# Optimization experiments

Measured on AMD Instinct MI355X. Metric: run time of the kernel, lower is better.

## Reference

```python
import jax, jax.numpy as jnp
import numpy as np

B, T, A, H, E = 256, 64, 32, 512, 32


def setup_inputs() -> dict:
    key = jax.random.key(0)
    ks = jax.random.split(key, 8)
    return {
        "actions": jax.random.normal(ks[0], (B, T, A), dtype=jnp.float32),
        "timesteps": jax.random.randint(ks[1], (B,), 0, 1000, dtype=jnp.int32),
        "cat_ids": jax.random.randint(ks[2], (B,), 0, E, dtype=jnp.int32),
        "W1": 0.02 * jax.random.normal(ks[3], (E, A, H), dtype=jnp.float32),
        "b1": jnp.zeros((E, H), dtype=jnp.float32),
        "W2": 0.02 * jax.random.normal(ks[4], (E, 2 * H, H), dtype=jnp.float32),
        "b2": jnp.zeros((E, H), dtype=jnp.float32),
        "W3": 0.02 * jax.random.normal(ks[5], (E, H, H), dtype=jnp.float32),
        "b3": jnp.zeros((E, H), dtype=jnp.float32),
    }


def _cat_linear(x, cat_ids, W, b):
    # per-sample weight gather + bmm, faithful to torch W[cat_ids]; bmm
    return jnp.einsum("btd,bdh->bth", x, W[cat_ids]) + b[cat_ids][:, None, :]


def _sinusoidal(timesteps_bt, dim):
    half = dim // 2
    exponent = -jnp.arange(half, dtype=jnp.float32) * (jnp.log(jnp.float32(10000.0)) / half)
    freqs = timesteps_bt[..., None] * jnp.exp(exponent)  # (B,T,half)
    return jnp.concatenate([jnp.sin(freqs), jnp.cos(freqs)], axis=-1)


def _swish(x):
    return x * jax.nn.sigmoid(x)


def reference(actions, timesteps, cat_ids, W1, b1, W2, b2, W3, b3):
    Bb, Tt, _ = actions.shape
    t_bt = jnp.broadcast_to(timesteps.astype(jnp.float32)[:, None], (Bb, Tt))
    a_emb = _cat_linear(actions, cat_ids, W1, b1)                     # (B,T,H)
    tau_emb = _sinusoidal(t_bt, a_emb.shape[-1]).astype(a_emb.dtype)  # (B,T,H)
    x = jnp.concatenate([a_emb, tau_emb], axis=-1)                    # (B,T,2H)
    x = _swish(_cat_linear(x, cat_ids, W2, b2))
    return _cat_linear(x, cat_ids, W3, b3)
```

## Files before the change

kernel.cpp:

```cpp
#include <hip/hip_runtime.h>
#include <hip/hip_bf16.h>

#define NB 256
#define NT 64
#define NA 32
#define NH 512
#define NE 32
#define MAXTILES 144

typedef short short8 __attribute__((ext_vector_type(8)));
typedef unsigned short ushort8v __attribute__((ext_vector_type(8)));
typedef float f32x4 __attribute__((ext_vector_type(4)));

__device__ __forceinline__ unsigned short f2bf(float f) {
  unsigned int u = __float_as_uint(f);
  u += 0x7FFFu + ((u >> 16) & 1u);
  return (unsigned short)(u >> 16);
}

__device__ __forceinline__ void gl2lds16(const void* g, void* l) {
  __builtin_amdgcn_global_load_lds(
      (const __attribute__((address_space(1))) unsigned int*)g,
      (__attribute__((address_space(3))) unsigned int*)l, 16, 0, 0);
}

__device__ __forceinline__ ushort8v cvt8(float4 a, float4 b) {
  ushort8v t;
  t[0] = f2bf(a.x); t[1] = f2bf(a.y); t[2] = f2bf(a.z); t[3] = f2bf(a.w);
  t[4] = f2bf(b.x); t[5] = f2bf(b.y); t[6] = f2bf(b.z); t[7] = f2bf(b.w);
  return t;
}

__global__ __launch_bounds__(256) void groupk(const int* __restrict__ cat,
                                              int* __restrict__ tiles,
                                              int* __restrict__ ntiles_out,
                                              int* __restrict__ orderG,
                                              int* __restrict__ offG,
                                              int* __restrict__ cntG) {
  __shared__ int cnt[NE], off[NE], cur[NE];
  __shared__ int order[NB];
  int tid = threadIdx.x;
  if (tid < NE) cnt[tid] = 0;
  __syncthreads();
  int e = cat[tid];
  atomicAdd(&cnt[e], 1);
  __syncthreads();
  if (tid == 0) {
    int s = 0;
    for (int i = 0; i < NE; i++) { off[i] = s; cur[i] = s; s += cnt[i]; }
  }
  __syncthreads();
  int p = atomicAdd(&cur[e], 1);
  order[p] = tid;
  __syncthreads();
  orderG[tid] = order[tid];
  if (tid < NE) { offG[tid] = off[tid]; cntG[tid] = cnt[tid]; }
  if (tid == 0) {
    int nt = 0;
    for (int i = 0; i < NE; i++) {
      for (int j = 0; j < cnt[i]; j += 2) {
        tiles[3 * nt + 0] = i;
        tiles[3 * nt + 1] = order[off[i] + j];
        tiles[3 * nt + 2] = (j + 1 < cnt[i]) ? order[off[i] + j + 1] : -1;
        nt++;
      }
    }
    *ntiles_out = nt;
  }
}

__global__ __launch_bounds__(256) void prep_kernel(const float* __restrict__ W,
                                                   unsigned short* __restrict__ Wt,
                                                   int K) {
  __shared__ float S[64 * 66];
  int e = blockIdx.z;
  int nt = blockIdx.x * 64;
  int kt = blockIdx.y * 64;
  int TK = (K - kt) < 64 ? (K - kt) : 64;
  int tid = threadIdx.x;
  int units = TK * 32;
  for (int u = tid; u < units; u += 256) {
    int k = u >> 5, c = u & 31;
    float2 v = *(const float2*)(W + ((size_t)e * K + kt + k) * NH + nt + 2 * c);
    *(float2*)(&S[k * 66 + 2 * c]) = v;
  }
  __syncthreads();
  int csh = (TK == 64) ? 3 : 2;
  int CHm = (1 << csh) - 1;
  int wunits = 64 << csh;
  for (int u = tid; u < wunits; u += 256) {
    int n = u >> csh, c = u & CHm;
    ushort8v pk;
#pragma unroll
    for (int j = 0; j < 8; j++) pk[j] = f2bf(S[(c * 8 + j) * 66 + n]);
    *(ushort8v*)(Wt + ((size_t)e * NH + nt + n) * K + kt + c * 8) = pk;
  }
}

__device__ __forceinline__ void pf_w2(float2 (&pf)[8], const float* __restrict__ W2en,
                                      int k0, int tid) {
#pragma unroll
  for (int j = 0; j < 8; j++) {
    int u = j * 256 + tid;
    int kk = u >> 5, cc = u & 31;
    pf[j] = *(const float2*)(W2en + ((size_t)(k0 + kk) << 9) + cc * 2);
  }
}

__device__ __forceinline__ void pf_w1(float4 (&pfw)[2], const float* __restrict__ W1e,
                                      int k0, int tid) {
  int a = tid >> 3, p = tid & 7;
  const float* src = W1e + (size_t)a * NH + k0 + p * 8;
  pfw[0] = *(const float4*)src;
  pfw[1] = *(const float4*)(src + 4);
}

__device__ __forceinline__ void tau_stage(unsigned short* tauS,
                                          const int* __restrict__ timesteps,
                                          const int* __restrict__ orderG,
                                          int off, int c, int sg, int tid) {
  const float kLog = 0.035977893400931146f;
  for (int j = 0; j < 32; j++) {
    int u = j * 256 + tid;
    int s = u >> 9, k = u & 511;
    int si = sg * 16 + s;
    float t = (si < c) ? (float)timesteps[orderG[off + si]] : 0.f;
    float f = expf(-(float)(k & 255) * kLog);
    float ang = t * f;
    tauS[s * 520 + k] = f2bf((k < 256) ? sinf(ang) : cosf(ang));
  }
}

__global__ __launch_bounds__(256) void w2fuse_kernel(
    const float* __restrict__ W1, const float* __restrict__ b1,
    const float* __restrict__ W2, const float* __restrict__ b2,
    const int* __restrict__ timesteps, const int* __restrict__ orderG,
    const int* __restrict__ offG, const int* __restrict__ cntG,
    unsigned short* __restrict__ Wt12, float* __restrict__ tvec) {
  __shared__ __align__(16) float S[64 * 66];
  __shared__ __align__(16) unsigned short Bs[64 * 64];
  __shared__ __align__(16) unsigned short As[32 * 64];
  __shared__ __align__(16) unsigned short tauS[16 * 520];
  __shared__ __align__(16) float b1S[512];
  __shared__ __align__(16) float bias2P[64 * 8];
  __shared__ __align__(16) float bias2S[64];

  int tid = threadIdx.x;
  int e = blockIdx.y, n0 = blockIdx.x * 64;
  int w = tid >> 6, l = tid & 63;
  int lrow = l & 15, kq = l >> 4;
  int tn = tid & 63, tp = tid >> 6;
  int c = cntG[e], off = offG[e];

  const float* W2en = W2 + ((size_t)e << 19) + n0;
  const float* W1e = W1 + ((size_t)e << 14);

  {
    float2 v = *(const float2*)(b1 + (size_t)e * NH + tid * 2);
    *(float2*)(&b1S[tid * 2]) = v;
  }
  tau_stage(tauS, timesteps, orderG, off, c, 0, tid);

  float2 pf[2][8];
  float4 pfW[2][2];
  pf_w2(pf[0], W2en, 0, tid);
  pf_w1(pfW[0], W1e, 0, tid);

  f32x4 acc1[2];
  acc1[0] = (f32x4){0.f, 0.f, 0.f, 0.f};
  acc1[1] = (f32x4){0.f, 0.f, 0.f, 0.f};
  f32x4 acc2 = (f32x4){0.f, 0.f, 0.f, 0.f};
  float bacc0 = 0.f, bacc1 = 0.f;

#pragma unroll
  for (int chunk = 0; chunk < 16; chunk++) {
    const int cur = chunk & 1, nxt = cur ^ 1;
    __syncthreads();
#pragma unroll
    for (int j = 0; j < 8; j++) {
      int u = j * 256 + tid;
      int kk = u >> 5, cc = u & 31;
      *(float2*)(&S[kk * 66 + cc * 2]) = pf[cur][j];
    }
    if (chunk < 15) pf_w2(pf[nxt], W2en, (chunk + 1) * 64, tid);
    if (chunk < 8) {
      int a = tid >> 3, p = tid & 7;
      *(ushort8v*)(&As[a * 64 + (p ^ (a & 7)) * 8]) = cvt8(pfW[cur][0], pfW[cur][1]);
      if (chunk < 7) pf_w1(pfW[nxt], W1e, (chunk + 1) * 64, tid);
    }
    __syncthreads();
#pragma unroll
    for (int i2 = 0; i2 < 2; i2++) {
      int p = tp + i2 * 4;
      ushort8v pk;
      float bsum = 0.f;
#pragma unroll
      for (int jj = 0; jj < 8; jj++) {
        float sv = S[(p * 8 + jj) * 66 + tn];
        pk[jj] = f2bf(sv);
        if (chunk < 8) bsum += sv * b1S[chunk * 64 + p * 8 + jj];
      }
      *(ushort8v*)(&Bs[tn * 64 + (p ^ (tn & 7)) * 8]) = pk;
      if (chunk < 8) { if (i2 == 0) bacc0 += bsum; else bacc1 += bsum; }
    }
    __syncthreads();
    if (chunk < 8) {
#pragma unroll
      for (int s2 = 0; s2 < 2; s2++) {
        int nrow = w * 16 + lrow;
        short8 bf = *(short8*)(&Bs[nrow * 64 + (((s2 * 4 + kq) ^ (nrow & 7))) * 8]);
#pragma unroll
        for (int mi = 0; mi < 2; mi++) {
          int ar = mi * 16 + lrow;
          short8 af = *(short8*)(&As[ar * 64 + (((s2 * 4 + kq) ^ (ar & 7))) * 8]);
          acc1[mi] = __builtin_amdgcn_mfma_f32_16x16x32_bf16(af, bf, acc1[mi], 0, 0, 0);
        }
      }
    } else {
#pragma unroll
      for (int s2 = 0; s2 < 2; s2++) {
        int nrow = w * 16 + lrow;
        short8 bf = *(short8*)(&Bs[nrow * 64 + (((s2 * 4 + kq) ^ (nrow & 7))) * 8]);
        short8 af = *(short8*)(&tauS[lrow * 520 + (chunk - 8) * 64 + s2 * 32 + kq * 8]);
        acc2 = __builtin_amdgcn_mfma_f32_16x16x32_bf16(af, bf, acc2, 0, 0, 0);
      }
    }
  }

  unsigned short* Sb = (unsigned short*)S;
#pragma unroll
  for (int mi = 0; mi < 2; mi++)
#pragma unroll
    for (int r = 0; r < 4; r++)
      Sb[(w * 16 + lrow) * 40 + mi * 16 + kq * 4 + r] = f2bf(acc1[mi][r]);
  bias2P[tn * 8 + tp] = bacc0;
  bias2P[tn * 8 + tp + 4] = bacc1;
  __syncthreads();
  if (tid < 64) {
    float s = b2[(size_t)e * NH + n0 + tid];
#pragma unroll
    for (int p2 = 0; p2 < 8; p2++) s += bias2P[tid * 8 + p2];
    bias2S[tid] = s;
  }
  {
    int n = tid >> 2, q = tid & 3;
    ushort8v v = *(ushort8v*)(&Sb[n * 40 + q * 8]);
    *(ushort8v*)(Wt12 + ((size_t)(e * NH) + n0 + n) * NA + q * 8) = v;
  }
  __syncthreads();

  {
    float bb = bias2S[w * 16 + lrow];
#pragma unroll
    for (int r = 0; r < 4; r++) {
      int si = kq * 4 + r;
      if (si < c)
        tvec[(size_t)orderG[off + si] * NH + n0 + w * 16 + lrow] = acc2[r] + bb;
    }
  }

  for (int sg = 1; sg * 16 < c; sg++) {
    __syncthreads();
    tau_stage(tauS, timesteps, orderG, off, c, sg, tid);
    pf_w2(pf[0], W2en, 512, tid);
    f32x4 acc2b = (f32x4){0.f, 0.f, 0.f, 0.f};
#pragma unroll
    for (int chunk = 8; chunk < 16; chunk++) {
      const int cur = chunk & 1, nxt = cur ^ 1;
      __syncthreads();
#pragma unroll
      for (int j = 0; j < 8; j++) {
        int u = j * 256 + tid;
        int kk = u >> 5, cc = u & 31;
        *(float2*)(&S[kk * 66 + cc * 2]) = pf[cur][j];
      }
      if (chunk < 15) pf_w2(pf[nxt], W2en, (chunk + 1) * 64, tid);
      __syncthreads();
#pragma unroll
      for (int i2 = 0; i2 < 2; i2++) {
        int p = tp + i2 * 4;
        ushort8v pk;
#pragma unroll
        for (int jj = 0; jj < 8; jj++) pk[jj] = f2bf(S[(p * 8 + jj) * 66 + tn]);
        *(ushort8v*)(&Bs[tn * 64 + (p ^ (tn & 7)) * 8]) = pk;
      }
      __syncthreads();
#pragma unroll
      for (int s2 = 0; s2 < 2; s2++) {
        int nrow = w * 16 + lrow;
        short8 bf = *(short8*)(&Bs[nrow * 64 + (((s2 * 4 + kq) ^ (nrow & 7))) * 8]);
        short8 af = *(short8*)(&tauS[lrow * 520 + (chunk - 8) * 64 + s2 * 32 + kq * 8]);
        acc2b = __builtin_amdgcn_mfma_f32_16x16x32_bf16(af, bf, acc2b, 0, 0, 0);
      }
    }
    float bb = bias2S[w * 16 + lrow];
#pragma unroll
    for (int r = 0; r < 4; r++) {
      int si = sg * 16 + kq * 4 + r;
      if (si < c)
        tvec[(size_t)orderG[off + si] * NH + n0 + w * 16 + lrow] = acc2b[r] + bb;
    }
  }
}

__global__ __launch_bounds__(256) void gemmh_kernel(
    const float* __restrict__ actions, const unsigned short* __restrict__ Wt12,
    const float* __restrict__ tvec, const int* __restrict__ cat_ids,
    unsigned short* __restrict__ Hb) {
  __shared__ __align__(16) unsigned char smem[16384 + 5120 + 33792];
  unsigned short* Ws = (unsigned short*)smem;
  unsigned short* As = (unsigned short*)(smem + 16384);
  unsigned short* Ts = (unsigned short*)(smem + 16384 + 5120);

  int b = blockIdx.y, h = blockIdx.x;
  int tid = threadIdx.x;
  int e = cat_ids[b];

  {
    const unsigned short* wsrc = Wt12 + ((size_t)e * NH + h * 256) * NA;
#pragma unroll
    for (int j = 0; j < 4; j++) {
      int u = j * 256 + tid;
      int n = u >> 2, p = u & 3;
      int ch = p ^ ((n >> 1) & 3);
      gl2lds16(wsrc + (size_t)n * NA + ch * 8,
               Ws + (size_t)(j * 256 + (tid & 448)) * 8);
    }
  }
  {
    int row = tid >> 2, seg = tid & 3;
    const float* src = actions + (size_t)(b * NT + row) * NA + seg * 8;
    float4 v0 = *(const float4*)(src);
    float4 v1 = *(const float4*)(src + 4);
    *(ushort8v*)(&As[row * 40 + seg * 8]) = cvt8(v0, v1);
  }
  __syncthreads();

  int w = tid >> 6, l = tid & 63;
  int lrow = l & 15, kq = l >> 4;
  short8 af = *(short8*)(&As[(w * 16 + lrow) * 40 + kq * 8]);
  f32x4 zero = {0.f, 0.f, 0.f, 0.f};
  f32x4 acc[16];
#pragma unroll
  for (int ni = 0; ni < 16; ni++) {
    int nn = ni * 16 + lrow;
    int p = kq ^ ((nn >> 1) & 3);
    short8 bfv = *(short8*)(&Ws[nn * 32 + p * 8]);
    acc[ni] = __builtin_amdgcn_mfma_f32_16x16x32_bf16(af, bfv, zero, 0, 0, 0);
  }
#pragma unroll
  for (int ni = 0; ni < 16; ni++) {
    int colL = ni * 16 + lrow;
    float bv = tvec[(size_t)b * NH + h * 256 + colL];
#pragma unroll
    for (int r = 0; r < 4; r++) {
      int row = w * 16 + kq * 4 + r;
      float v = acc[ni][r] + bv;
      v = v / (1.0f + __expf(-v));
      Ts[row * 264 + colL] = f2bf(v);
    }
  }
  __syncthreads();
#pragma unroll
  for (int i = 0; i < 8; i++) {
    int u = i * 256 + tid;
    int t = u >> 5, c4 = u & 31;
    uint4 v = *(uint4*)(&Ts[t * 264 + c4 * 8]);
    *(uint4*)(Hb + ((size_t)(b * NT + t)) * NH + h * 256 + c4 * 8) = v;
  }
}

template <int KTOT, bool HASTAU, bool SWISH, bool OUT_BF16>
__global__ __launch_bounds__(256) void gemm2_kernel(
    const unsigned short* __restrict__ Xa, const unsigned short* __restrict__ Xt,
    const unsigned short* __restrict__ Wt, const float* __restrict__ bias,
    void* __restrict__ Yv, const int* __restrict__ tiles,
    const int* __restrict__ pntiles) {
  constexpr int SMEM = OUT_BF16 ? 24576 : 34816;
  __shared__ __align__(16) unsigned char smem[SMEM];
  unsigned short* As = (unsigned short*)smem;
  unsigned short* Bs = (unsigned short*)(smem + 16384);

  int ti = blockIdx.y;
  if (ti >= *pntiles) return;
  int n0 = blockIdx.x * 64;
  int e = tiles[3 * ti], s0 = tiles[3 * ti + 1], s1 = tiles[3 * ti + 2];
  int s1v = (s1 < 0) ? s0 : s1;

  int tid = threadIdx.x;
  int l = tid & 63;
  int wr = (tid >> 7), wc = (tid >> 6) & 1;
  int lrow = l & 15, kq = l >> 4;

  f32x4 acc[4][2];
#pragma unroll
  for (int mi = 0; mi < 4; mi++)
#pragma unroll
    for (int ni = 0; ni < 2; ni++) acc[mi][ni] = (f32x4){0.f, 0.f, 0.f, 0.f};

  const unsigned short* wbase = Wt + ((size_t)e * NH + n0) * KTOT;

  for (int it = 0; it < KTOT / 64; it++) {
    int k0 = it * 64;
    __syncthreads();
#pragma unroll
    for (int j = 0; j < 4; j++) {
      int u = j * 256 + tid;
      int row = u >> 3, p = u & 7;
      int ch = p ^ (row & 7);
      int kk = k0 + ch * 8;
      int s = (row < 64) ? s0 : s1v;
      const unsigned short* src;
      if (HASTAU && kk >= 512)
        src = Xt + (size_t)s * NH + (kk - 512);
      else
        src = Xa + ((size_t)(s * NT + (row & 63))) * NH + kk;
      gl2lds16(src, As + (size_t)(j * 256 + (tid & 448)) * 8);
    }
#pragma unroll
    for (int j = 0; j < 2; j++) {
      int u = j * 256 + tid;
      int n = u >> 3, p = u & 7;
      int ch = p ^ (n & 7);
      gl2lds16(wbase + (size_t)n * KTOT + k0 + ch * 8,
               Bs + (size_t)(j * 256 + (tid & 448)) * 8);
    }
    __syncthreads();

    short8 afr[2][4], bfr[2][2];
#pragma unroll
    for (int s2 = 0; s2 < 2; s2++) {
#pragma unroll
      for (int mi = 0; mi < 4; mi++) {
        int row = wr * 64 + mi * 16 + lrow;
        int p = (s2 * 4 + kq) ^ (row & 7);
        afr[s2][mi] = *(short8*)(&As[row * 64 + p * 8]);
      }
#pragma unroll
      for (int ni = 0; ni < 2; ni++) {
        int n = wc * 32 + ni * 16 + lrow;
        int p = (s2 * 4 + kq) ^ (n & 7);
        bfr[s2][ni] = *(short8*)(&Bs[n * 64 + p * 8]);
      }
    }
#pragma unroll
    for (int s2 = 0; s2 < 2; s2++)
#pragma unroll
      for (int mi = 0; mi < 4; mi++)
#pragma unroll
        for (int ni = 0; ni < 2; ni++)
          acc[mi][ni] = __builtin_amdgcn_mfma_f32_16x16x32_bf16(
              afr[s2][mi], bfr[s2][ni], acc[mi][ni], 0, 0, 0);
  }
  __syncthreads();

#pragma unroll
  for (int ni = 0; ni < 2; ni++) {
    int colL = wc * 32 + ni * 16 + lrow;
    float bv = bias[(size_t)e * NH + n0 + colL];
#pragma unroll
    for (int mi = 0; mi < 4; mi++) {
#pragma unroll
      for (int r = 0; r < 4; r++) {
        int row = wr * 64 + mi * 16 + kq * 4 + r;
        float v = acc[mi][ni][r] + bv;
        if (SWISH) v = v / (1.0f + __expf(-v));
        if (OUT_BF16)
          ((unsigned short*)smem)[row * 80 + colL] = f2bf(v);
        else
          ((float*)smem)[row * 68 + colL] = v;
      }
    }
  }
  __syncthreads();
  if (OUT_BF16) {
    unsigned short* Y = (unsigned short*)Yv;
#pragma unroll
    for (int i = 0; i < 4; i++) {
      int u = i * 256 + tid;
      int row = u >> 3, c = u & 7;
      if (row >= 64 && s1 < 0) continue;
      int s = (row < 64) ? s0 : s1;
      uint4 v = *(uint4*)(&((unsigned short*)smem)[row * 80 + c * 8]);
      *(uint4*)(Y + ((size_t)(s * NT + (row & 63))) * NH + n0 + c * 8) = v;
    }
  } else {
    float* Y = (float*)Yv;
#pragma unroll
    for (int i = 0; i < 8; i++) {
      int u = i * 256 + tid;
      int row = u >> 4, c = u & 15;
      if (row >= 64 && s1 < 0) continue;
      int s = (row < 64) ? s0 : s1;
      uint4 v = *(uint4*)(&((float*)smem)[row * 68 + c * 4]);
      *(uint4*)(Y + ((size_t)(s * NT + (row & 63))) * NH + n0 + c * 4) = v;
    }
  }
}

extern "C" void kernel_launch(void* const* d_in, const int* in_sizes, int n_in,
                              void* d_out, int out_size, void* d_ws, size_t ws_size,
                              hipStream_t stream) {
  const float* actions   = (const float*)d_in[0];
  const int*   timesteps = (const int*)d_in[1];
  const int*   cat_ids   = (const int*)d_in[2];
  const float* W1 = (const float*)d_in[3];
  const float* b1 = (const float*)d_in[4];
  const float* W2 = (const float*)d_in[5];
  const float* b2 = (const float*)d_in[6];
  const float* W3 = (const float*)d_in[7];
  const float* b3 = (const float*)d_in[8];

  unsigned short* Hb   = (unsigned short*)d_ws;
  unsigned short* Wt3  = (unsigned short*)((char*)d_ws + (size_t)16777216);
  unsigned short* Wt12 = (unsigned short*)((char*)d_ws + (size_t)33554432);
  float* tvec  = (float*)((char*)d_ws + (size_t)34603008);
  int* tiles   = (int*)((char*)d_ws + (size_t)35192832);
  int* ntiles  = tiles + 3 * MAXTILES;
  int* orderG  = ntiles + 1;
  int* offG    = orderG + NB;
  int* cntG    = offG + NE;

  groupk<<<1, 256, 0, stream>>>(cat_ids, tiles, ntiles, orderG, offG, cntG);
  w2fuse_kernel<<<dim3(8, NE), 256, 0, stream>>>(W1, b1, W2, b2, timesteps,
                                                 orderG, offG, cntG, Wt12, tvec);
  prep_kernel<<<dim3(8, 8, NE), 256, 0, stream>>>(W3, Wt3, 512);
  gemmh_kernel<<<dim3(2, NB), 256, 0, stream>>>(actions, Wt12, tvec, cat_ids, Hb);
  gemm2_kernel<512, false, false, false><<<dim3(8, MAXTILES), 256, 0, stream>>>(
      Hb, nullptr, Wt3, b3, d_out, tiles, ntiles);
}
```

Baseline: 212.6 us.

## Merge W3 prep into weight-fusion kernel and double-buffer gemm2 LDS loads

Folds the W3 transpose/bf16 conversion into the W1·W2 fusion kernel as extra blocks, removing a separate launch and letting both preprocessing jobs overlap. Rewrites the final gemm2 main loop to use two LDS buffers with async global-to-LDS prefetch two stages ahead, with explicit vmcnt/lgkmcnt waits and barriers. Larger shared memory usage may lower occupancy of gemm2 and the merged kernel.

After: 202.6 us. 1.05x faster.

```diff
diff --git a/kernel.cpp b/kernel.cpp
--- a/kernel.cpp
+++ b/kernel.cpp
@@ -66,34 +66,6 @@
       }
     }
     *ntiles_out = nt;
-  }
-}
-
-__global__ __launch_bounds__(256) void prep_kernel(const float* __restrict__ W,
-                                                   unsigned short* __restrict__ Wt,
-                                                   int K) {
-  __shared__ float S[64 * 66];
-  int e = blockIdx.z;
-  int nt = blockIdx.x * 64;
-  int kt = blockIdx.y * 64;
-  int TK = (K - kt) < 64 ? (K - kt) : 64;
-  int tid = threadIdx.x;
-  int units = TK * 32;
-  for (int u = tid; u < units; u += 256) {
-    int k = u >> 5, c = u & 31;
-    float2 v = *(const float2*)(W + ((size_t)e * K + kt + k) * NH + nt + 2 * c);
-    *(float2*)(&S[k * 66 + 2 * c]) = v;
-  }
-  __syncthreads();
-  int csh = (TK == 64) ? 3 : 2;
-  int CHm = (1 << csh) - 1;
-  int wunits = 64 << csh;
-  for (int u = tid; u < wunits; u += 256) {
-    int n = u >> csh, c = u & CHm;
-    ushort8v pk;
-#pragma unroll
-    for (int j = 0; j < 8; j++) pk[j] = f2bf(S[(c * 8 + j) * 66 + n]);
-    *(ushort8v*)(Wt + ((size_t)e * NH + nt + n) * K + kt + c * 8) = pk;
   }
 }
 
@@ -131,22 +103,51 @@
   }
 }
 
-__global__ __launch_bounds__(256) void w2fuse_kernel(
+__global__ __launch_bounds__(256) void wp_kernel(
     const float* __restrict__ W1, const float* __restrict__ b1,
     const float* __restrict__ W2, const float* __restrict__ b2,
     const int* __restrict__ timesteps, const int* __restrict__ orderG,
     const int* __restrict__ offG, const int* __restrict__ cntG,
-    unsigned short* __restrict__ Wt12, float* __restrict__ tvec) {
-  __shared__ __align__(16) float S[64 * 66];
-  __shared__ __align__(16) unsigned short Bs[64 * 64];
-  __shared__ __align__(16) unsigned short As[32 * 64];
-  __shared__ __align__(16) unsigned short tauS[16 * 520];
-  __shared__ __align__(16) float b1S[512];
-  __shared__ __align__(16) float bias2P[64 * 8];
-  __shared__ __align__(16) float bias2S[64];
-
+    unsigned short* __restrict__ Wt12, float* __restrict__ tvec,
+    const float* __restrict__ W3, unsigned short* __restrict__ Wt3) {
+  __shared__ __align__(16) unsigned char smem[50176];
   int tid = threadIdx.x;
-  int e = blockIdx.y, n0 = blockIdx.x * 64;
+
+  if (blockIdx.x >= 256) {
+    float* S = (float*)smem;
+    int id = blockIdx.x - 256;
+    int e = id >> 6, rem = id & 63;
+    int nt = (rem & 7) * 64, kt = (rem >> 3) * 64;
+#pragma unroll
+    for (int j = 0; j < 8; j++) {
+      int u = j * 256 + tid;
+      int k = u >> 5, c = u & 31;
+      float2 v = *(const float2*)(W3 + ((size_t)e * 512 + kt + k) * NH + nt + 2 * c);
+      *(float2*)(&S[k * 66 + 2 * c]) = v;
+    }
+    __syncthreads();
+#pragma unroll
+    for (int j = 0; j < 2; j++) {
+      int u = j * 256 + tid;
+      int n = u >> 3, c = u & 7;
+      ushort8v pk;
+#pragma unroll
+      for (int jj = 0; jj < 8; jj++) pk[jj] = f2bf(S[(c * 8 + jj) * 66 + n]);
+      *(ushort8v*)(Wt3 + ((size_t)e * NH + nt + n) * 512 + kt + c * 8) = pk;
+    }
+    return;
+  }
+
+  float* S            = (float*)smem;
+  unsigned short* Bs  = (unsigned short*)(smem + 16896);
+  unsigned short* As  = (unsigned short*)(smem + 25088);
+  unsigned short* tauS= (unsigned short*)(smem + 29184);
+  float* b1S          = (float*)(smem + 45824);
+  float* bias2P       = (float*)(smem + 47872);
+  float* bias2S       = (float*)(smem + 49920);
+
+  int bxx = blockIdx.x;
+  int e = bxx >> 3, n0 = (bxx & 7) * 64;
   int w = tid >> 6, l = tid & 63;
   int lrow = l & 15, kq = l >> 4;
   int tn = tid & 63, tp = tid >> 6;
@@ -376,10 +377,7 @@
     const unsigned short* __restrict__ Wt, const float* __restrict__ bias,
     void* __restrict__ Yv, const int* __restrict__ tiles,
     const int* __restrict__ pntiles) {
-  constexpr int SMEM = OUT_BF16 ? 24576 : 34816;
-  __shared__ __align__(16) unsigned char smem[SMEM];
-  unsigned short* As = (unsigned short*)smem;
-  unsigned short* Bs = (unsigned short*)(smem + 16384);
+  __shared__ __align__(16) unsigned char smem[49152];
 
   int ti = blockIdx.y;
   if (ti >= *pntiles) return;
@@ -392,17 +390,13 @@
   int wr = (tid >> 7), wc = (tid >> 6) & 1;
   int lrow = l & 15, kq = l >> 4;
 
-  f32x4 acc[4][2];
-#pragma unroll
-  for (int mi = 0; mi < 4; mi++)
-#pragma unroll
-    for (int ni = 0; ni < 2; ni++) acc[mi][ni] = (f32x4){0.f, 0.f, 0.f, 0.f};
-
   const unsigned short* wbase = Wt + ((size_t)e * NH + n0) * KTOT;
-
-  for (int it = 0; it < KTOT / 64; it++) {
+  constexpr int NIT = KTOT / 64;
+
+  auto stage = [&](int it, int buf) {
+    unsigned short* As = (unsigned short*)(smem + buf * 24576);
+    unsigned short* Bs = (unsigned short*)(smem + buf * 24576 + 16384);
     int k0 = it * 64;
-    __syncthreads();
 #pragma unroll
     for (int j = 0; j < 4; j++) {
       int u = j * 256 + tid;
@@ -425,7 +419,30 @@
       gl2lds16(wbase + (size_t)n * KTOT + k0 + ch * 8,
                Bs + (size_t)(j * 256 + (tid & 448)) * 8);
     }
-    __syncthreads();
+  };
+
+  f32x4 acc[4][2];
+#pragma unroll
+  for (int mi = 0; mi < 4; mi++)
+#pragma unroll
+    for (int ni = 0; ni < 2; ni++) acc[mi][ni] = (f32x4){0.f, 0.f, 0.f, 0.f};
+
+  stage(0, 0);
+  stage(1, 1);
+
+  for (int t = 0; t < NIT; t++) {
+    int cur = t & 1;
+    unsigned short* As = (unsigned short*)(smem + cur * 24576);
+    unsigned short* Bs = (unsigned short*)(smem + cur * 24576 + 16384);
+
+    if (t + 1 < NIT) {
+      asm volatile("s_waitcnt vmcnt(6)" ::: "memory");
+    } else {
+      asm volatile("s_waitcnt vmcnt(0)" ::: "memory");
+    }
+    __builtin_amdgcn_sched_barrier(0);
+    __builtin_amdgcn_s_barrier();
+    __builtin_amdgcn_sched_barrier(0);
 
     short8 afr[2][4], bfr[2][2];
 #pragma unroll
@@ -443,6 +460,13 @@
         bfr[s2][ni] = *(short8*)(&Bs[n * 64 + p * 8]);
       }
     }
+    asm volatile("s_waitcnt lgkmcnt(0)" ::: "memory");
+    __builtin_amdgcn_sched_barrier(0);
+    __builtin_amdgcn_s_barrier();
+    __builtin_amdgcn_sched_barrier(0);
+
+    if (t + 2 < NIT) stage(t + 2, cur);
+
 #pragma unroll
     for (int s2 = 0; s2 < 2; s2++)
 #pragma unroll
@@ -522,9 +546,8 @@
   int* cntG    = offG + NE;
 
   groupk<<<1, 256, 0, stream>>>(cat_ids, tiles, ntiles, orderG, offG, cntG);
-  w2fuse_kernel<<<dim3(8, NE), 256, 0, stream>>>(W1, b1, W2, b2, timesteps,
-                                                 orderG, offG, cntG, Wt12, tvec);
-  prep_kernel<<<dim3(8, 8, NE), 256, 0, stream>>>(W3, Wt3, 512);
+  wp_kernel<<<2304, 256, 0, stream>>>(W1, b1, W2, b2, timesteps, orderG, offG,
+                                      cntG, Wt12, tvec, W3, Wt3);
   gemmh_kernel<<<dim3(2, NB), 256, 0, stream>>>(actions, Wt12, tvec, cat_ids, Hb);
   gemm2_kernel<512, false, false, false><<<dim3(8, MAXTILES), 256, 0, stream>>>(
       Hb, nullptr, Wt3, b3, d_out, tiles, ntiles);
```
